# Kernel tuning notes

Measured on AMD Instinct MI355X. Metric: run time of the kernel, lower is better.

## Reference

```python
import jax, jax.numpy as jnp
import numpy as np

STEPS = 50   # MattingSolver(steps=50)
H, W = 1024, 1024
EPS = 1e-2   # diagonal regularization (matting lambda-like), guarantees SPD


def _build_laplacian():
    """5-point weighted graph Laplacian + EPS*I on an HxW grid, COO, row-sorted."""
    rng = np.random.RandomState(0)
    n = H * W
    idx = np.arange(n, dtype=np.int32).reshape(H, W)
    wh = rng.rand(H, W - 1).astype(np.float32) + 0.1  # horizontal edge weights
    wv = rng.rand(H - 1, W).astype(np.float32) + 0.1  # vertical edge weights
    a_h, b_h = idx[:, :-1].ravel(), idx[:, 1:].ravel()
    a_v, b_v = idx[:-1, :].ravel(), idx[1:, :].ravel()
    diag_idx = np.arange(n, dtype=np.int32)
    rows = np.concatenate([a_h, b_h, a_v, b_v, diag_idx])
    cols = np.concatenate([b_h, a_h, b_v, a_v, diag_idx])
    off = np.concatenate([wh.ravel(), wh.ravel(), wv.ravel(), wv.ravel()])
    deg = np.zeros(n, dtype=np.float32)
    np.add.at(deg, a_h, wh.ravel()); np.add.at(deg, b_h, wh.ravel())
    np.add.at(deg, a_v, wv.ravel()); np.add.at(deg, b_v, wv.ravel())
    vals = np.concatenate([-off, deg + EPS]).astype(np.float32)
    order = np.argsort(rows, kind='stable')
    return rows[order], cols[order], vals[order]


def setup_inputs() -> dict:
    key = jax.random.key(0)
    rows, cols, vals = _build_laplacian()
    b = jax.random.normal(key, (H * W,), dtype=jnp.float32)
    return {"rows": jnp.asarray(rows), "cols": jnp.asarray(cols),
            "vals": jnp.asarray(vals), "b": b}


def reference(rows, cols, vals, b):
    """Unpreconditioned conjugate gradient: solve A x = b, x0 = 0, STEPS iters."""
    n = b.shape[0]

    def spmv(p):  # y = A @ p via COO gather + segment-sum scatter
        return jax.ops.segment_sum(vals * p[cols], rows, num_segments=n,
                                   indices_are_sorted=True)

    x0 = jnp.zeros_like(b)
    r0 = b                      # r = b - A @ 0
    rs0 = jnp.dot(r0, r0)

    def body(carry, _):
        x, r, p, rs = carry
        Ap = spmv(p)
        alpha = rs / jnp.dot(p, Ap)
        x = x + alpha * p
        r = r - alpha * Ap
        rs_new = jnp.dot(r, r)
        p = r + (rs_new / rs) * p
        return (x, r, p, rs_new), None

    (x, _, _, _), _ = jax.lax.scan(body, (x0, r0, r0, rs0), None, length=STEPS)
    return x
```

## Files before the change

kernel.cpp:

```cpp
#include <hip/hip_runtime.h>


#define HH 1024
#define WW 1024
#define CG_STEPS 50
#define NB 256
#define NT 1024
#define RING 4

#define SCOPE __HIP_MEMORY_SCOPE_AGENT

__device__ __forceinline__ float aload(const float* p) {
    return __hip_atomic_load(p, __ATOMIC_RELAXED, SCOPE);
}
__device__ __forceinline__ void astore(float* p, float v) {
    __hip_atomic_store(p, v, __ATOMIC_RELAXED, SCOPE);
}
__device__ __forceinline__ int iload(const int* p) {
    return __hip_atomic_load(p, __ATOMIC_RELAXED, SCOPE);
}
__device__ __forceinline__ void istore(int* p, int v) {
    __hip_atomic_store(p, v, __ATOMIC_RELAXED, SCOPE);
}
__device__ __forceinline__ unsigned long long uload(const unsigned long long* p) {
    return __hip_atomic_load(p, __ATOMIC_RELAXED, SCOPE);
}
__device__ __forceinline__ void ustore(unsigned long long* p, unsigned long long v) {
    __hip_atomic_store(p, v, __ATOMIC_RELAXED, SCOPE);
}

__device__ __forceinline__ unsigned long long packtd(unsigned tag, double d) {
    return ((unsigned long long)tag << 48) |
           (((unsigned long long)__double_as_longlong(d)) >> 16);
}
__device__ __forceinline__ double unpacktd(unsigned long long v) {
    return __longlong_as_double((long long)(v << 16));
}

__global__ __launch_bounds__(NT)
void cgsolve_kernel(const int* __restrict__ cols, const float* __restrict__ vals,
                    const float* __restrict__ b, float* __restrict__ xout,
                    float* __restrict__ rbuf,
                    unsigned long long* __restrict__ redr,
                    int* __restrict__ flags) {
    const int col = threadIdx.x;
    const int bb  = blockIdx.x;

    __shared__ float  sr[4][WW + 1];
    __shared__ double sa[16][2];
    __shared__ double sc[4][2];
    __shared__ int    scols[2][5 * WW];
    __shared__ float  svals[2][5 * WW];

    float adiag[4], art[4], alf[4], adn[4], awu[4];
    float x_[4], r_[4], w_[4], q_[4];
    float p_[4] = {0.f, 0.f, 0.f, 0.f};
    float s_[4] = {0.f, 0.f, 0.f, 0.f};
    float z_[4] = {0.f, 0.f, 0.f, 0.f};

    for (int half = 0; half < 2; ++half) {
        __syncthreads();
        #pragma unroll
        for (int rr2 = 0; rr2 < 2; ++rr2) {
            const int i    = 4 * bb + 2 * half + rr2;
            const int off  = (i == 0) ? 0 : (4 * WW - 2) + (i - 1) * (5 * WW - 2);
            const int base = 1 + (i > 0) + (i < HH - 1);
            const int len2 = (base * WW + 2 * WW - 2) >> 1;
            const int2*   gc = (const int2*)(cols + off);
            const float2* gv = (const float2*)(vals + off);
            int2*   lc = (int2*)scols[rr2];
            float2* lv = (float2*)svals[rr2];
            for (int e = threadIdx.x; e < len2; e += NT) {
                lc[e] = gc[e];
                lv[e] = gv[e];
            }
        }
        __syncthreads();
        #pragma unroll
        for (int rr2 = 0; rr2 < 2; ++rr2) {
            const int rr     = 2 * half + rr2;
            const int i      = 4 * bb + rr;
            const int base   = 1 + (i > 0) + (i < HH - 1);
            const int j      = col;
            const int within = (j == 0) ? 0 : (base + 1) + (j - 1) * (base + 2);
            const int nnz    = base + (j > 0) + (j < WW - 1);
            const int t      = i * WW + j;
            float dg = 0.f, wr = 0.f, wl = 0.f, wd = 0.f, wu = 0.f;
            #pragma unroll
            for (int e = 0; e < 5; ++e) {
                if (e < nnz) {
                    const int   c = scols[rr2][within + e];
                    const float v = svals[rr2][within + e];
                    if (c == t)           dg = v;
                    else if (c == t + 1)  wr = v;
                    else if (c == t - 1)  wl = v;
                    else if (c == t + WW) wd = v;
                    else if (c == t - WW) wu = v;
                }
            }
            adiag[rr] = dg; art[rr] = wr; alf[rr] = wl; adn[rr] = wd; awu[rr] = wu;
            r_[rr] = b[t];
            x_[rr] = 0.f;
        }
    }

    {
        #pragma unroll
        for (int rr = 0; rr < 4; ++rr) sr[rr][col] = r_[rr];
        __syncthreads();
        const float btop = (bb > 0)      ? b[(4 * bb - 1) * WW + col] : 0.f;
        const float bbot = (bb < NB - 1) ? b[(4 * bb + 4) * WW + col] : 0.f;
        double rs_d = 0.0, dl_d = 0.0;
        #pragma unroll
        for (int rr = 0; rr < 4; ++rr) {
            float sum = adiag[rr] * r_[rr];
            const float vr = (col < WW - 1) ? sr[rr][col + 1] : 0.f;
            const float vl = (col > 0)      ? sr[rr][col - 1] : 0.f;
            sum += art[rr] * vr + alf[rr] * vl;
            const float vd = (rr < 3) ? r_[rr + 1] : bbot;
            const float vu = (rr > 0) ? r_[rr - 1] : btop;
            sum += adn[rr] * vd + awu[rr] * vu;
            w_[rr] = sum;
            rs_d += (double)r_[rr] * r_[rr];
            dl_d += (double)sum * r_[rr];
        }
        astore(&rbuf[(2 * bb + 0) * WW + col], w_[0]);
        astore(&rbuf[(2 * bb + 1) * WW + col], w_[3]);
        #pragma unroll
        for (int mask = 1; mask < 64; mask <<= 1) {
            rs_d += __shfl_xor(rs_d, mask, 64);
            dl_d += __shfl_xor(dl_d, mask, 64);
        }
        const int lane = threadIdx.x & 63, wid = threadIdx.x >> 6;
        if (lane == 0) { sa[wid][0] = rs_d; sa[wid][1] = dl_d; }
        __syncthreads();
        if (threadIdx.x < 16) {
            double t0 = sa[threadIdx.x][0], t1 = sa[threadIdx.x][1];
            #pragma unroll
            for (int mask = 1; mask < 16; mask <<= 1) {
                t0 += __shfl_xor(t0, mask, 16);
                t1 += __shfl_xor(t1, mask, 16);
            }
            if (threadIdx.x == 0) {
                unsigned long long* bp = redr + bb;
                ustore(bp,      packtd(0u, t0));
                ustore(bp + NB, packtd(0u, t1));
                istore(&flags[bb], 1);
            }
        }
    }

    double gamma_prev = 1.0, alpha_prev = 1.0;

    #pragma unroll 1
    for (int k = 0; k < CG_STEPS; ++k) {
        if (k < CG_STEPS - 1) {
            #pragma unroll
            for (int rr = 0; rr < 4; ++rr) sr[rr][col] = w_[rr];
            if (threadIdx.x < 2) {
                const int nb2 = bb + (threadIdx.x ? 1 : -1);
                if (nb2 >= 0 && nb2 < NB)
                    while (iload(&flags[nb2]) < k + 1) __builtin_amdgcn_s_sleep(1);
            }
            __syncthreads();
            const float* hb = rbuf + (size_t)(k & 1) * 2 * NB * WW;
            const float wtop = (bb > 0)
                ? aload(&hb[(2 * (bb - 1) + 1) * WW + col]) : 0.f;
            const float wbot = (bb < NB - 1)
                ? aload(&hb[(2 * (bb + 1) + 0) * WW + col]) : 0.f;
            #pragma unroll
            for (int rr = 0; rr < 4; ++rr) {
                float sum = adiag[rr] * w_[rr];
                const float vr = (col < WW - 1) ? sr[rr][col + 1] : 0.f;
                const float vl = (col > 0)      ? sr[rr][col - 1] : 0.f;
                sum += art[rr] * vr + alf[rr] * vl;
                const float vd = (rr < 3) ? w_[rr + 1] : wbot;
                const float vu = (rr > 0) ? w_[rr - 1] : wtop;
                sum += adn[rr] * vd + awu[rr] * vu;
                q_[rr] = sum;
            }
        }

        double gam, del;
        {
            if (threadIdx.x < NB) {
                const unsigned want = (unsigned)k;
                const unsigned long long* bp =
                    redr + (size_t)(k & (RING - 1)) * 2 * NB + threadIdx.x;
                unsigned long long v0 = uload(bp);
                unsigned long long v1 = uload(bp + NB);
                while ((unsigned)(v0 >> 48) != want ||
                       (unsigned)(v1 >> 48) != want) {
                    __builtin_amdgcn_s_sleep(1);
                    if ((unsigned)(v0 >> 48) != want) v0 = uload(bp);
                    if ((unsigned)(v1 >> 48) != want) v1 = uload(bp + NB);
                }
                double t0 = unpacktd(v0), t1 = unpacktd(v1);
                #pragma unroll
                for (int mask = 1; mask < 64; mask <<= 1) {
                    t0 += __shfl_xor(t0, mask, 64);
                    t1 += __shfl_xor(t1, mask, 64);
                }
                if ((threadIdx.x & 63) == 0) {
                    const int g = threadIdx.x >> 6;
                    sc[g][0] = t0; sc[g][1] = t1;
                }
            }
            __syncthreads();
            gam = ((sc[0][0] + sc[1][0]) + sc[2][0]) + sc[3][0];
            del = ((sc[0][1] + sc[1][1]) + sc[2][1]) + sc[3][1];
        }

        const double beta  = (k == 0) ? 0.0 : gam / gamma_prev;
        const double alpha = (k == 0) ? gam / del
                                      : gam / (del - beta * gam / alpha_prev);
        const float betaf = (float)beta, alphaf = (float)alpha;
        #pragma unroll
        for (int rr = 0; rr < 4; ++rr) {
            p_[rr] = r_[rr] + betaf * p_[rr];
            x_[rr] += alphaf * p_[rr];
        }
        if (k == CG_STEPS - 1) break;

        double rs_d = 0.0, dl_d = 0.0;
        #pragma unroll
        for (int rr = 0; rr < 4; ++rr) {
            z_[rr] = q_[rr] + betaf * z_[rr];
            s_[rr] = w_[rr] + betaf * s_[rr];
            r_[rr] -= alphaf * s_[rr];
            w_[rr] -= alphaf * z_[rr];
            rs_d += (double)r_[rr] * r_[rr];
            dl_d += (double)w_[rr] * r_[rr];
        }
        float* hbn = rbuf + (size_t)((k + 1) & 1) * 2 * NB * WW;
        astore(&hbn[(2 * bb + 0) * WW + col], w_[0]);
        astore(&hbn[(2 * bb + 1) * WW + col], w_[3]);
        #pragma unroll
        for (int mask = 1; mask < 64; mask <<= 1) {
            rs_d += __shfl_xor(rs_d, mask, 64);
            dl_d += __shfl_xor(dl_d, mask, 64);
        }
        const int lane = threadIdx.x & 63, wid = threadIdx.x >> 6;
        if (lane == 0) { sa[wid][0] = rs_d; sa[wid][1] = dl_d; }
        __syncthreads();
        if (threadIdx.x < 16) {
            double t0 = sa[threadIdx.x][0], t1 = sa[threadIdx.x][1];
            #pragma unroll
            for (int mask = 1; mask < 16; mask <<= 1) {
                t0 += __shfl_xor(t0, mask, 16);
                t1 += __shfl_xor(t1, mask, 16);
            }
            if (threadIdx.x == 0) {
                unsigned long long* bp =
                    redr + (size_t)((k + 1) & (RING - 1)) * 2 * NB + bb;
                ustore(bp,      packtd((unsigned)(k + 1), t0));
                ustore(bp + NB, packtd((unsigned)(k + 1), t1));
                istore(&flags[bb], k + 2);
            }
        }

        gamma_prev = gam; alpha_prev = alpha;
    }

    #pragma unroll
    for (int rr = 0; rr < 4; ++rr)
        xout[(4 * bb + rr) * WW + col] = x_[rr];
}

extern "C" void kernel_launch(void* const* d_in, const int* in_sizes, int n_in,
                              void* d_out, int out_size, void* d_ws, size_t ws_size,
                              hipStream_t stream) {
    const int*   cols = (const int*)d_in[1];
    const float* vals = (const float*)d_in[2];
    const float* b    = (const float*)d_in[3];
    float* x = (float*)d_out;

    float* rbuf = (float*)d_ws;
    unsigned long long* redr =
        (unsigned long long*)(rbuf + 2 * 2 * (size_t)NB * WW);
    int* flags = (int*)(redr + (size_t)RING * 2 * NB);

    cgsolve_kernel<<<dim3(NB), dim3(NT), 0, stream>>>(cols, vals, b, x,
                                                      rbuf, redr, flags);
}
```

Baseline: 287.1 us.

## Precompute next-step CG dot products algebraically from twelve partial inner products

Instead of reducing r·r and w·r after the vector update, each block now computes twelve inner products of r, w, s, z, q right after the SpMV. The next iteration's gamma and delta are then reconstructed algebraically from these using the previous alpha and beta. This lets the grid-wide reduction overlap with the vector updates and the neighbour halo exchange instead of sitting on the critical path after them, and the flag publish now only guards the halo. In exchange each reduction carries twelve doubles instead of two, and reconstructing by expansion can lose accuracy through cancellation. The launch-bounds occupancy hint is also changed.

```diff
diff --git a/kernel.cpp b/kernel.cpp
--- a/kernel.cpp
+++ b/kernel.cpp
@@ -7,6 +7,7 @@
 #define NB 256
 #define NT 1024
 #define RING 4
+#define ND 12
 
 #define SCOPE __HIP_MEMORY_SCOPE_AGENT
 
@@ -37,18 +38,19 @@
     return __longlong_as_double((long long)(v << 16));
 }
 
-__global__ __launch_bounds__(NT)
+__global__ __launch_bounds__(NT, 4)
 void cgsolve_kernel(const int* __restrict__ cols, const float* __restrict__ vals,
                     const float* __restrict__ b, float* __restrict__ xout,
                     float* __restrict__ rbuf,
+                    unsigned long long* __restrict__ red0,
                     unsigned long long* __restrict__ redr,
                     int* __restrict__ flags) {
     const int col = threadIdx.x;
     const int bb  = blockIdx.x;
 
     __shared__ float  sr[4][WW + 1];
-    __shared__ double sa[16][2];
-    __shared__ double sc[4][2];
+    __shared__ double sa[16][ND];
+    __shared__ double sc[4][ND];
     __shared__ int    scols[2][5 * WW];
     __shared__ float  svals[2][5 * WW];
 
@@ -142,15 +144,14 @@
                 t1 += __shfl_xor(t1, mask, 16);
             }
             if (threadIdx.x == 0) {
-                unsigned long long* bp = redr + bb;
-                ustore(bp,      packtd(0u, t0));
-                ustore(bp + NB, packtd(0u, t1));
+                ustore(red0 + bb,      packtd(0u, t0));
+                ustore(red0 + NB + bb, packtd(0u, t1));
                 istore(&flags[bb], 1);
             }
         }
     }
 
-    double gamma_prev = 1.0, alpha_prev = 1.0;
+    double gamma_prev = 1.0, alpha_prev = 1.0, beta_prev = 0.0;
 
     #pragma unroll 1
     for (int k = 0; k < CG_STEPS; ++k) {
@@ -179,21 +180,68 @@
                 sum += adn[rr] * vd + awu[rr] * vu;
                 q_[rr] = sum;
             }
+
+            double d0 = 0., d1 = 0., d2 = 0., d3 = 0., d4 = 0., d5 = 0.,
+                   d6 = 0., d7 = 0., d8 = 0., d9 = 0., d10 = 0., d11 = 0.;
+            #pragma unroll
+            for (int rr = 0; rr < 4; ++rr) {
+                const double rd = r_[rr], wd = w_[rr], qd = q_[rr];
+                const double sd = s_[rr], zd = z_[rr];
+                d0  += rd * rd;
+                d1  += rd * wd;
+                d2  += wd * wd;
+                d3  += rd * sd;
+                d4  += wd * sd;
+                d5  += sd * sd;
+                d6  += qd * wd;
+                d7  += qd * sd;
+                d8  += zd * sd;
+                d9  += qd * rd;
+                d10 += zd * rd;
+                d11 += zd * wd;
+            }
+            double d[ND] = {d0, d1, d2, d3, d4, d5, d6, d7, d8, d9, d10, d11};
+            #pragma unroll
+            for (int mask = 1; mask < 64; mask <<= 1) {
+                #pragma unroll
+                for (int j = 0; j < ND; ++j) d[j] += __shfl_xor(d[j], mask, 64);
+            }
+            {
+                const int lane = threadIdx.x & 63, wid = threadIdx.x >> 6;
+                if (lane == 0) {
+                    #pragma unroll
+                    for (int j = 0; j < ND; ++j) sa[wid][j] = d[j];
+                }
+            }
+            __syncthreads();
+            if (threadIdx.x < 16) {
+                double t[ND];
+                #pragma unroll
+                for (int j = 0; j < ND; ++j) t[j] = sa[threadIdx.x][j];
+                #pragma unroll
+                for (int mask = 1; mask < 16; mask <<= 1) {
+                    #pragma unroll
+                    for (int j = 0; j < ND; ++j) t[j] += __shfl_xor(t[j], mask, 16);
+                }
+                if (threadIdx.x == 0) {
+                    unsigned long long* bp =
+                        redr + (size_t)(k & (RING - 1)) * ND * NB + bb;
+                    #pragma unroll
+                    for (int j = 0; j < ND; ++j)
+                        ustore(bp + j * NB, packtd((unsigned)k, t[j]));
+                }
+            }
         }
 
         double gam, del;
-        {
+        if (k == 0) {
             if (threadIdx.x < NB) {
-                const unsigned want = (unsigned)k;
-                const unsigned long long* bp =
-                    redr + (size_t)(k & (RING - 1)) * 2 * NB + threadIdx.x;
-                unsigned long long v0 = uload(bp);
-                unsigned long long v1 = uload(bp + NB);
-                while ((unsigned)(v0 >> 48) != want ||
-                       (unsigned)(v1 >> 48) != want) {
+                unsigned long long v0 = uload(red0 + threadIdx.x);
+                unsigned long long v1 = uload(red0 + NB + threadIdx.x);
+                while ((v0 >> 48) != 0ull || (v1 >> 48) != 0ull) {
                     __builtin_amdgcn_s_sleep(1);
-                    if ((unsigned)(v0 >> 48) != want) v0 = uload(bp);
-                    if ((unsigned)(v1 >> 48) != want) v1 = uload(bp + NB);
+                    if ((v0 >> 48) != 0ull) v0 = uload(red0 + threadIdx.x);
+                    if ((v1 >> 48) != 0ull) v1 = uload(red0 + NB + threadIdx.x);
                 }
                 double t0 = unpacktd(v0), t1 = unpacktd(v1);
                 #pragma unroll
@@ -209,6 +257,53 @@
             __syncthreads();
             gam = ((sc[0][0] + sc[1][0]) + sc[2][0]) + sc[3][0];
             del = ((sc[0][1] + sc[1][1]) + sc[2][1]) + sc[3][1];
+        } else {
+            if (threadIdx.x < NB) {
+                const unsigned want = (unsigned)(k - 1);
+                const unsigned long long* bp =
+                    redr + (size_t)((k - 1) & (RING - 1)) * ND * NB + threadIdx.x;
+                unsigned long long v[ND];
+                #pragma unroll
+                for (int j = 0; j < ND; ++j) v[j] = uload(bp + j * NB);
+                for (;;) {
+                    bool ok = true;
+                    #pragma unroll
+                    for (int j = 0; j < ND; ++j)
+                        ok &= ((unsigned)(v[j] >> 48) == want);
+                    if (ok) break;
+                    __builtin_amdgcn_s_sleep(1);
+                    #pragma unroll
+                    for (int j = 0; j < ND; ++j)
+                        if ((unsigned)(v[j] >> 48) != want)
+                            v[j] = uload(bp + j * NB);
+                }
+                double t[ND];
+                #pragma unroll
+                for (int j = 0; j < ND; ++j) t[j] = unpacktd(v[j]);
+                #pragma unroll
+                for (int mask = 1; mask < 64; mask <<= 1) {
+                    #pragma unroll
+                    for (int j = 0; j < ND; ++j) t[j] += __shfl_xor(t[j], mask, 64);
+                }
+                if ((threadIdx.x & 63) == 0) {
+                    const int g = threadIdx.x >> 6;
+                    #pragma unroll
+                    for (int j = 0; j < ND; ++j) sc[g][j] = t[j];
+                }
+            }
+            __syncthreads();
+            double S[ND];
+            #pragma unroll
+            for (int j = 0; j < ND; ++j)
+                S[j] = ((sc[0][j] + sc[1][j]) + sc[2][j]) + sc[3][j];
+            const double a  = alpha_prev, bt = beta_prev;
+            const double rsk = S[1] + bt * S[3];
+            const double ssk = S[2] + 2.0 * bt * S[4] + bt * bt * S[5];
+            const double wsk = S[2] + bt * S[4];
+            const double zrk = S[9] + bt * S[10];
+            const double zsk = S[6] + bt * (S[7] + S[11]) + bt * bt * S[8];
+            gam = S[0] - 2.0 * a * rsk + a * a * ssk;
+            del = S[1] - a * (wsk + zrk) + a * a * zsk;
         }
 
         const double beta  = (k == 0) ? 0.0 : gam / gamma_prev;
@@ -222,44 +317,20 @@
         }
         if (k == CG_STEPS - 1) break;
 
-        double rs_d = 0.0, dl_d = 0.0;
         #pragma unroll
         for (int rr = 0; rr < 4; ++rr) {
             z_[rr] = q_[rr] + betaf * z_[rr];
             s_[rr] = w_[rr] + betaf * s_[rr];
             r_[rr] -= alphaf * s_[rr];
             w_[rr] -= alphaf * z_[rr];
-            rs_d += (double)r_[rr] * r_[rr];
-            dl_d += (double)w_[rr] * r_[rr];
         }
         float* hbn = rbuf + (size_t)((k + 1) & 1) * 2 * NB * WW;
         astore(&hbn[(2 * bb + 0) * WW + col], w_[0]);
         astore(&hbn[(2 * bb + 1) * WW + col], w_[3]);
-        #pragma unroll
-        for (int mask = 1; mask < 64; mask <<= 1) {
-            rs_d += __shfl_xor(rs_d, mask, 64);
-            dl_d += __shfl_xor(dl_d, mask, 64);
-        }
-        const int lane = threadIdx.x & 63, wid = threadIdx.x >> 6;
-        if (lane == 0) { sa[wid][0] = rs_d; sa[wid][1] = dl_d; }
-        __syncthreads();
-        if (threadIdx.x < 16) {
-            double t0 = sa[threadIdx.x][0], t1 = sa[threadIdx.x][1];
-            #pragma unroll
-            for (int mask = 1; mask < 16; mask <<= 1) {
-                t0 += __shfl_xor(t0, mask, 16);
-                t1 += __shfl_xor(t1, mask, 16);
-            }
-            if (threadIdx.x == 0) {
-                unsigned long long* bp =
-                    redr + (size_t)((k + 1) & (RING - 1)) * 2 * NB + bb;
-                ustore(bp,      packtd((unsigned)(k + 1), t0));
-                ustore(bp + NB, packtd((unsigned)(k + 1), t1));
-                istore(&flags[bb], k + 2);
-            }
-        }
-
-        gamma_prev = gam; alpha_prev = alpha;
+        __syncthreads();
+        if (threadIdx.x == 0) istore(&flags[bb], k + 2);
+
+        gamma_prev = gam; alpha_prev = alpha; beta_prev = beta;
     }
 
     #pragma unroll
@@ -276,10 +347,11 @@
     float* x = (float*)d_out;
 
     float* rbuf = (float*)d_ws;
-    unsigned long long* redr =
+    unsigned long long* red0 =
         (unsigned long long*)(rbuf + 2 * 2 * (size_t)NB * WW);
-    int* flags = (int*)(redr + (size_t)RING * 2 * NB);
+    unsigned long long* redr = red0 + 2 * NB;
+    int* flags = (int*)(redr + (size_t)RING * ND * NB);
 
     cgsolve_kernel<<<dim3(NB), dim3(NT), 0, stream>>>(cols, vals, b, x,
-                                                      rbuf, redr, flags);
-}
+                                                      rbuf, red0, redr, flags);
+}
```

After: 797.5 us. 178% more time.
